# Optimization experiments

Hardware: AMD Instinct MI355X
Metric: run time of the kernel (lower is better)

The kernel has to match this reference:

```python
import jax, jax.numpy as jnp
import numpy as np

N_NODES = 50000
N_EDGES = 800000
N_GRAPHS = 128
HIDDEN = 64
HEADS = 2
OUT = 4
NEG_SLOPE = 0.2
ALPHA_FLAG = 0.05


def _gat_conv(x, src, dst, W, a_src, a_dst, b):
    # PyG GATConv, concat=False (mean over heads), self-loops already appended.
    N = x.shape[0]
    H, C = a_src.shape
    xh = (x @ W).reshape(N, H, C)                       # [N,H,C]
    s_src = (xh * a_src).sum(-1)                        # [N,H]
    s_dst = (xh * a_dst).sum(-1)                        # [N,H]
    e = s_src[src] + s_dst[dst]                         # [E,H]
    e = jnp.where(e > 0, e, NEG_SLOPE * e)              # LeakyReLU(0.2)
    emax = jax.ops.segment_max(e, dst, num_segments=N)  # per-dst softmax max
    emax = jnp.where(jnp.isfinite(emax), emax, 0.0)
    p = jnp.exp(e - emax[dst])
    denom = jax.ops.segment_sum(p, dst, num_segments=N)
    alpha = p / (denom[dst] + 1e-16)                    # [E,H]
    out = jax.ops.segment_sum(alpha[:, :, None] * xh[src], dst, num_segments=N)
    return out.mean(axis=1) + b                         # [N,HIDDEN]


def setup_inputs() -> dict:
    key = jax.random.key(0)
    ks = jax.random.split(key, 32)
    f = lambda k, shape, s=0.1: (jax.random.normal(k, shape) * s).astype(jnp.float32)
    inp = {}
    inp['x_all'] = jax.random.normal(ks[0], (N_NODES, 8), dtype=jnp.float32)
    inp['climber'] = jax.random.normal(ks[1], (N_GRAPHS, 4), dtype=jnp.float32)
    inp['edge_index'] = jax.random.randint(ks[2], (2, N_EDGES), 0, N_NODES)
    inp['batch'] = jnp.sort(jax.random.randint(ks[3], (N_NODES,), 0, N_GRAPHS))
    H = HIDDEN
    inp['W_in'] = f(ks[4], (6, H)); inp['b_in'] = jnp.zeros((H,), jnp.float32)
    inp['W_c'] = f(ks[5], (4, H)); inp['b_c'] = jnp.zeros((H,), jnp.float32)
    inp['W_f1'] = f(ks[6], (H, 2 * H)); inp['b_f1'] = jnp.zeros((2 * H,), jnp.float32)
    inp['W_f2'] = f(ks[7], (H, 2 * H)); inp['b_f2'] = jnp.zeros((2 * H,), jnp.float32)
    inp['W_g1'] = f(ks[8], (H, HEADS * H)); inp['a_src1'] = f(ks[9], (HEADS, H)); inp['a_dst1'] = f(ks[10], (HEADS, H)); inp['b_g1'] = jnp.zeros((H,), jnp.float32)
    inp['W_g2'] = f(ks[11], (H, HEADS * H)); inp['a_src2'] = f(ks[12], (HEADS, H)); inp['a_dst2'] = f(ks[13], (HEADS, H)); inp['b_g2'] = jnp.zeros((H,), jnp.float32)
    inp['W_cl1'] = f(ks[14], (H, H)); inp['b_cl1'] = jnp.zeros((H,), jnp.float32)
    inp['W_cl2'] = f(ks[15], (H, OUT)); inp['b_cl2'] = jnp.zeros((OUT,), jnp.float32)
    inp['W_fh1'] = f(ks[16], (2, 8), 0.001); inp['b_fh1'] = jnp.zeros((8,), jnp.float32)
    inp['W_fh2'] = f(ks[17], (8, OUT), 0.001); inp['b_fh2'] = jnp.zeros((OUT,), jnp.float32)
    return inp


def reference(x_all, climber, edge_index, batch, W_in, b_in, W_c, b_c,
              W_f1, b_f1, W_f2, b_f2,
              W_g1, a_src1, a_dst1, b_g1,
              W_g2, a_src2, a_dst2, b_g2,
              W_cl1, b_cl1, W_cl2, b_cl2,
              W_fh1, b_fh1, W_fh2, b_fh2):
    N = x_all.shape[0]
    flags = x_all[:, -2:]
    x = x_all[:, :-2]
    # climber embedding (eval mode -> dropout is identity)
    c = jax.nn.relu(climber @ W_c + b_c)                 # [G,H]
    x = x @ W_in + b_in                                  # [N,H]
    # FiLM 1
    gb = c @ W_f1 + b_f1
    gamma, beta = jnp.split(gb, 2, axis=-1)
    x = x * (1.0 + gamma[batch]) + beta[batch]
    # add self-loops (PyG GATConv default)
    loop = jnp.arange(N, dtype=edge_index.dtype)
    src = jnp.concatenate([edge_index[0], loop])
    dst = jnp.concatenate([edge_index[1], loop])
    x = jax.nn.relu(_gat_conv(x, src, dst, W_g1, a_src1, a_dst1, b_g1))
    # FiLM 2
    gb = c @ W_f2 + b_f2
    gamma, beta = jnp.split(gb, 2, axis=-1)
    x = x * (1.0 + gamma[batch]) + beta[batch]
    x = jax.nn.relu(_gat_conv(x, src, dst, W_g2, a_src2, a_dst2, b_g2))
    logits_main = jax.nn.relu(x @ W_cl1 + b_cl1) @ W_cl2 + b_cl2
    logits_flag = jax.nn.relu(flags @ W_fh1 + b_fh1) @ W_fh2 + b_fh2
    return logits_main + ALPHA_FLAG * logits_flag
```

## Files before the change

### kernel.cpp

```cpp
#include <hip/hip_runtime.h>
#include <hip/hip_fp16.h>

#define NEG_SLOPE 0.2f
#define ALPHA_FLAG 0.05f

typedef _Float16 h2t __attribute__((ext_vector_type(2)));
union h2u { unsigned u; h2t h; __half2 hh; float f; };
static __device__ __forceinline__ h2t u_as_h2(unsigned u) { h2u c; c.u = u; return c.h; }
static __device__ __forceinline__ float h2_as_f(__half2 h) { h2u c; c.hh = h; return c.f; }
static __device__ __forceinline__ h2t f_as_h2(float f) { h2u c; c.f = f; return c.h; }

static inline size_t align256(size_t x) { return (x + 255) & ~(size_t)255; }

__global__ void prep_kernel(const float* __restrict__ climber,
                            const float* __restrict__ W_c, const float* __restrict__ b_c,
                            const float* __restrict__ W_f1, const float* __restrict__ b_f1,
                            const float* __restrict__ W_f2, const float* __restrict__ b_f2,
                            float* __restrict__ gb1, float* __restrict__ gb2) {
    __shared__ float c_sh[64];
    int g = blockIdx.x, t = threadIdx.x;
    if (t < 64) {
        float acc = b_c[t];
#pragma unroll
        for (int k = 0; k < 4; ++k) acc = fmaf(climber[g * 4 + k], W_c[k * 64 + t], acc);
        c_sh[t] = fmaxf(acc, 0.f);
    }
    __syncthreads();
    float a1 = b_f1[t], a2 = b_f2[t];
#pragma unroll 8
    for (int h = 0; h < 64; ++h) {
        float cv = c_sh[h];
        a1 = fmaf(cv, W_f1[h * 128 + t], a1);
        a2 = fmaf(cv, W_f2[h * 128 + t], a2);
    }
    gb1[g * 128 + t] = a1;
    gb2[g * 128 + t] = a2;
}

__global__ void hist_kernel(const int* __restrict__ dst, int E, int* __restrict__ counts) {
    int i4 = (blockIdx.x * blockDim.x + threadIdx.x) * 4;
    if (i4 + 3 < E) {
        int4 d = *(const int4*)&dst[i4];
        atomicAdd(&counts[d.x], 1);
        atomicAdd(&counts[d.y], 1);
        atomicAdd(&counts[d.z], 1);
        atomicAdd(&counts[d.w], 1);
    } else {
        for (int u = 0; u < 4; ++u)
            if (i4 + u < E) atomicAdd(&counts[dst[i4 + u]], 1);
    }
}

#define SCAN_CHUNK 1024
__global__ void scan_partial_kernel(const int* __restrict__ counts, int* __restrict__ block_sums, int N) {
    __shared__ int sh[256];
    int b = blockIdx.x, t = threadIdx.x;
    int idx0 = b * SCAN_CHUNK + t * 4;
    int s = 0;
    if (idx0 + 3 < N) {
        int4 v = *(const int4*)&counts[idx0];
        s = v.x + v.y + v.z + v.w + 4;
    } else {
#pragma unroll
        for (int u = 0; u < 4; ++u) if (idx0 + u < N) s += counts[idx0 + u] + 1;
    }
    sh[t] = s;
    __syncthreads();
#pragma unroll
    for (int off = 128; off; off >>= 1) {
        if (t < off) sh[t] += sh[t + off];
        __syncthreads();
    }
    if (t == 0) block_sums[b] = sh[0];
}

__global__ void scan_final_kernel(const int* __restrict__ counts, const int* __restrict__ block_sums,
                                  int nb, int* __restrict__ row_ptr, int* __restrict__ fill, int N) {
    __shared__ int sh[256];
    __shared__ int base_sh;
    int b = blockIdx.x, t = threadIdx.x;
    if (t < 64) {
        int v = (t < nb && t < b) ? block_sums[t] : 0;
#pragma unroll
        for (int off = 32; off; off >>= 1) v += __shfl_xor(v, off);
        if (t == 0) base_sh = v;
    }
    int idx0 = b * SCAN_CHUNK + t * 4;
    int c[4];
    if (idx0 + 3 < N) {
        int4 v = *(const int4*)&counts[idx0];
        c[0] = v.x + 1; c[1] = v.y + 1; c[2] = v.z + 1; c[3] = v.w + 1;
    } else {
#pragma unroll
        for (int u = 0; u < 4; ++u) c[u] = (idx0 + u < N) ? counts[idx0 + u] + 1 : 0;
    }
    int s = c[0] + c[1] + c[2] + c[3];
    sh[t] = s;
    __syncthreads();
#pragma unroll
    for (int off = 1; off < 256; off <<= 1) {
        int add = (t >= off) ? sh[t - off] : 0;
        __syncthreads();
        sh[t] += add;
        __syncthreads();
    }
    int run = base_sh + sh[t] - s;
#pragma unroll
    for (int u = 0; u < 4; ++u) {
        if (idx0 + u < N) {
            row_ptr[idx0 + u] = run;
            fill[idx0 + u] = run;
            run += c[u];
            if (idx0 + u == N - 1) row_ptr[N] = run;
        }
    }
}

__global__ void scatter_kernel(const int* __restrict__ src, const int* __restrict__ dst,
                               int Eh, int N, int* __restrict__ fill, int* __restrict__ csr_src) {
    int t = blockIdx.x * blockDim.x + threadIdx.x;
    if (t < Eh) {
        int2 s2 = *(const int2*)&src[t * 2];
        int2 d2 = *(const int2*)&dst[t * 2];
        int p0 = atomicAdd(&fill[d2.x], 1); csr_src[p0] = s2.x;
        int p1 = atomicAdd(&fill[d2.y], 1); csr_src[p1] = s2.y;
    } else {
        int i = t - Eh;
        if (i < N) { int p = atomicAdd(&fill[i], 1); csr_src[p] = i; }
    }
}

#define XH_NB 32
__global__ __launch_bounds__(256, 4) void xh_kernel(
    const __half* __restrict__ xhalf, const float* __restrict__ W_g,
    const float* __restrict__ a_src, const float* __restrict__ a_dst,
    __half* __restrict__ xh, float* __restrict__ s_src, float* __restrict__ s_dst,
    int N, int in_mode,
    const float* __restrict__ x_all, const int* __restrict__ batch,
    const float* __restrict__ W_in, const float* __restrict__ b_in,
    const float* __restrict__ gb1) {
    __shared__ float x_sh[XH_NB * 64];
    __shared__ float win_sh[6 * 64 + 64];
    int t = threadIdx.x;
    int base = blockIdx.x * XH_NB;
    if (in_mode) {
        for (int i = t; i < 448; i += 256)
            win_sh[i] = (i < 384) ? W_in[i] : b_in[i - 384];
        __syncthreads();
        int nd = t >> 3;
        int jb = (t & 7) * 8;
        int n = base + nd;
        if (n < N) {
            float4 a = *(const float4*)&x_all[(size_t)n * 8];
            float2 b = *(const float2*)&x_all[(size_t)n * 8 + 4];
            float xa[6] = {a.x, a.y, a.z, a.w, b.x, b.y};
            int g = batch[n];
            const float* gbrow = &gb1[g * 128];
#pragma unroll
            for (int jj = 0; jj < 8; ++jj) {
                int j = jb + jj;
                float acc = win_sh[384 + j];
#pragma unroll
                for (int k = 0; k < 6; ++k) acc = fmaf(xa[k], win_sh[k * 64 + j], acc);
                x_sh[nd * 64 + j] = acc * (1.f + gbrow[j]) + gbrow[64 + j];
            }
        } else {
#pragma unroll
            for (int jj = 0; jj < 8; ++jj) x_sh[nd * 64 + jb + jj] = 0.f;
        }
    } else {
        int nvalid = N - base; if (nvalid > XH_NB) nvalid = XH_NB;
        int nhalves = nvalid * 64;
        int idx = t * 8;
        uint4 raw = make_uint4(0, 0, 0, 0);
        if (idx < nhalves) raw = *(const uint4*)&xhalf[(size_t)base * 64 + idx];
        float2 f0 = __half22float2(*(__half2*)&raw.x);
        float2 f1 = __half22float2(*(__half2*)&raw.y);
        float2 f2 = __half22float2(*(__half2*)&raw.z);
        float2 f3 = __half22float2(*(__half2*)&raw.w);
        x_sh[idx + 0] = f0.x; x_sh[idx + 1] = f0.y;
        x_sh[idx + 2] = f1.x; x_sh[idx + 3] = f1.y;
        x_sh[idx + 4] = f2.x; x_sh[idx + 5] = f2.y;
        x_sh[idx + 6] = f3.x; x_sh[idx + 7] = f3.y;
    }
    __syncthreads();
    int c = t & 63;
    int g = t >> 6;
    float acc0[8], acc1[8];
#pragma unroll
    for (int i = 0; i < 8; ++i) { acc0[i] = 0.f; acc1[i] = 0.f; }
    const float* W0 = W_g + c;
    const float* W1 = W_g + 64 + c;
#pragma unroll 2
    for (int k = 0; k < 64; k += 4) {
        float w0[4], w1[4];
#pragma unroll
        for (int u = 0; u < 4; ++u) { w0[u] = W0[(k + u) * 128]; w1[u] = W1[(k + u) * 128]; }
#pragma unroll
        for (int i = 0; i < 8; ++i) {
            float4 xv = *(const float4*)&x_sh[(g * 8 + i) * 64 + k];
            acc0[i] = fmaf(xv.x, w0[0], acc0[i]);
            acc0[i] = fmaf(xv.y, w0[1], acc0[i]);
            acc0[i] = fmaf(xv.z, w0[2], acc0[i]);
            acc0[i] = fmaf(xv.w, w0[3], acc0[i]);
            acc1[i] = fmaf(xv.x, w1[0], acc1[i]);
            acc1[i] = fmaf(xv.y, w1[1], acc1[i]);
            acc1[i] = fmaf(xv.z, w1[2], acc1[i]);
            acc1[i] = fmaf(xv.w, w1[3], acc1[i]);
        }
    }
    float as0 = a_src[c], ad0 = a_dst[c];
    float as1 = a_src[64 + c], ad1 = a_dst[64 + c];
#pragma unroll
    for (int i = 0; i < 8; ++i) {
        int n = base + g * 8 + i;
        float ps0 = acc0[i] * as0, pd0 = acc0[i] * ad0;
        float ps1 = acc1[i] * as1, pd1 = acc1[i] * ad1;
#pragma unroll
        for (int off = 32; off; off >>= 1) {
            ps0 += __shfl_xor(ps0, off); pd0 += __shfl_xor(pd0, off);
            ps1 += __shfl_xor(ps1, off); pd1 += __shfl_xor(pd1, off);
        }
        if (n < N) {
            if (c == 0) {
                s_src[n * 2 + 0] = ps0; s_src[n * 2 + 1] = ps1;
                s_dst[n * 2 + 0] = pd0; s_dst[n * 2 + 1] = pd1;
            }
            __half2 hv = __floats2half2_rn(acc0[i], acc1[i]);
            *(__half2*)&xh[(size_t)n * 128 + c * 2] = hv;
        }
    }
}

static __device__ __forceinline__ float dot2acc(unsigned xbits, h2t w, float acc) {
#if __has_builtin(__builtin_amdgcn_fdot2)
    return __builtin_amdgcn_fdot2(u_as_h2(xbits), w, acc, false);
#else
    h2u cx; cx.u = xbits;
    float2 xf = __half22float2(cx.hh);
    h2u cw; cw.h = w;
    float2 wf = __half22float2(cw.hh);
    return fmaf(xf.x, wf.x, fmaf(xf.y, wf.y, acc));
#endif
}

template <int MODE>
static __device__ __forceinline__ void agg_impl(
    const __half* __restrict__ xh, const float* __restrict__ s_src,
    const float* __restrict__ s_dst, const int* __restrict__ row_ptr,
    const int* __restrict__ csr_src, const float* __restrict__ b_g,
    const int* __restrict__ batch, const float* __restrict__ gb_film,
    __half* __restrict__ xout_h, int N,
    const float* __restrict__ x_all,
    const float* __restrict__ W_cl1, const float* __restrict__ b_cl1,
    const float* __restrict__ W_cl2, const float* __restrict__ b_cl2,
    const float* __restrict__ W_fh1, const float* __restrict__ b_fh1,
    const float* __restrict__ W_fh2, const float* __restrict__ b_fh2,
    float* __restrict__ out) {
    __shared__ float2 ps_sh[4][64];
    __shared__ float vh_sh[4][64];
    int lane = threadIdx.x & 63;
    int w = threadIdx.x >> 6;
    int n = (blockIdx.x * blockDim.x + threadIdx.x) >> 6;
    if (n >= N) return;
    int beg = row_ptr[n], end = row_ptr[n + 1];
    int deg = end - beg;
    float2 sd = *(const float2*)&s_dst[n * 2];
    const char* xhb = (const char*)xh;
    int sub = lane >> 4;
    unsigned q16 = (unsigned)(lane & 15) * 16u;
    float acc[4] = {0.f, 0.f, 0.f, 0.f};

    if (deg <= 64) {
        float p0 = 0.f, p1 = 0.f; unsigned sb = 0;
        if (lane < deg) {
            int s = csr_src[beg + lane];
            sb = (unsigned)s << 8;
            float2 ss = *(const float2*)&s_src[s * 2];
            float e0 = ss.x + sd.x, e1 = ss.y + sd.y;
            e0 = (e0 > 0.f) ? e0 : NEG_SLOPE * e0;
            e1 = (e1 > 0.f) ? e1 : NEG_SLOPE * e1;
            p0 = __expf(e0); p1 = __expf(e1);
        }
        float dp0 = p0, dp1 = p1;
#pragma unroll
        for (int off = 32; off; off >>= 1) {
            dp0 += __shfl_xor(dp0, off);
            dp1 += __shfl_xor(dp1, off);
        }
        float i0 = 0.5f / (dp0 + 1e-16f), i1 = 0.5f / (dp1 + 1e-16f);
        ps_sh[w][lane] = make_float2(h2_as_f(__floats2half2_rn(p0 * i0, p1 * i1)),
                                     __uint_as_float(sb));
        int mr = (deg + 3) & ~3;
        for (int j = 0; j < mr; j += 4) {
            float2 ps = ps_sh[w][j + sub];
            h2t wpk = f_as_h2(ps.x);
            unsigned voff = __float_as_uint(ps.y) + q16;
            uint4 hv = *(const uint4*)(xhb + voff);
            acc[0] = dot2acc(hv.x, wpk, acc[0]);
            acc[1] = dot2acc(hv.y, wpk, acc[1]);
            acc[2] = dot2acc(hv.z, wpk, acc[2]);
            acc[3] = dot2acc(hv.w, wpk, acc[3]);
        }
    } else {
        float dp0 = 0.f, dp1 = 0.f;
        for (int chunk = beg; chunk < end; chunk += 64) {
            int m = end - chunk; if (m > 64) m = 64;
            if (lane < m) {
                int s = csr_src[chunk + lane];
                float2 ss = *(const float2*)&s_src[s * 2];
                float e0 = ss.x + sd.x, e1 = ss.y + sd.y;
                e0 = (e0 > 0.f) ? e0 : NEG_SLOPE * e0;
                e1 = (e1 > 0.f) ? e1 : NEG_SLOPE * e1;
                dp0 += __expf(e0); dp1 += __expf(e1);
            }
        }
#pragma unroll
        for (int off = 32; off; off >>= 1) {
            dp0 += __shfl_xor(dp0, off);
            dp1 += __shfl_xor(dp1, off);
        }
        float i0 = 0.5f / (dp0 + 1e-16f), i1 = 0.5f / (dp1 + 1e-16f);
        for (int chunk = beg; chunk < end; chunk += 64) {
            int m = end - chunk; if (m > 64) m = 64;
            float p0 = 0.f, p1 = 0.f; unsigned sb = 0;
            if (lane < m) {
                int s = csr_src[chunk + lane];
                sb = (unsigned)s << 8;
                float2 ss = *(const float2*)&s_src[s * 2];
                float e0 = ss.x + sd.x, e1 = ss.y + sd.y;
                e0 = (e0 > 0.f) ? e0 : NEG_SLOPE * e0;
                e1 = (e1 > 0.f) ? e1 : NEG_SLOPE * e1;
                p0 = __expf(e0); p1 = __expf(e1);
            }
            ps_sh[w][lane] = make_float2(h2_as_f(__floats2half2_rn(p0 * i0, p1 * i1)),
                                         __uint_as_float(sb));
            int mr = (m + 3) & ~3;
            for (int j = 0; j < mr; j += 4) {
                float2 ps = ps_sh[w][j + sub];
                h2t wpk = f_as_h2(ps.x);
                unsigned voff = __float_as_uint(ps.y) + q16;
                uint4 hv = *(const uint4*)(xhb + voff);
                acc[0] = dot2acc(hv.x, wpk, acc[0]);
                acc[1] = dot2acc(hv.y, wpk, acc[1]);
                acc[2] = dot2acc(hv.z, wpk, acc[2]);
                acc[3] = dot2acc(hv.w, wpk, acc[3]);
            }
        }
    }
#pragma unroll
    for (int u = 0; u < 4; ++u) {
        acc[u] += __shfl_xor(acc[u], 16);
        acc[u] += __shfl_xor(acc[u], 32);
    }
    if (lane < 16) *(float4*)&vh_sh[w][lane * 4] = make_float4(acc[0], acc[1], acc[2], acc[3]);
    float v = vh_sh[w][lane] + b_g[lane];
    v = fmaxf(v, 0.f);
    if (MODE == 0) {
        int g = batch[n];
        v = v * (1.f + gb_film[g * 128 + lane]) + gb_film[g * 128 + 64 + lane];
        xout_h[(size_t)n * 64 + lane] = __float2half(v);
        return;
    }
    vh_sh[w][lane] = v;
    float h = b_cl1[lane];
#pragma unroll 4
    for (int k = 0; k < 64; k += 4) {
        float4 vq = *(const float4*)&vh_sh[w][k];
        h = fmaf(vq.x, W_cl1[(k + 0) * 64 + lane], h);
        h = fmaf(vq.y, W_cl1[(k + 1) * 64 + lane], h);
        h = fmaf(vq.z, W_cl1[(k + 2) * 64 + lane], h);
        h = fmaf(vq.w, W_cl1[(k + 3) * 64 + lane], h);
    }
    h = fmaxf(h, 0.f);
    float4 w2 = *(const float4*)&W_cl2[lane * 4];
    float o0 = h * w2.x, o1 = h * w2.y, o2 = h * w2.z, o3 = h * w2.w;
#pragma unroll
    for (int off = 32; off; off >>= 1) {
        o0 += __shfl_xor(o0, off); o1 += __shfl_xor(o1, off);
        o2 += __shfl_xor(o2, off); o3 += __shfl_xor(o3, off);
    }
    if (lane < 4) {
        float f0 = x_all[(size_t)n * 8 + 6], f1 = x_all[(size_t)n * 8 + 7];
        float lf = b_fh2[lane];
#pragma unroll
        for (int m = 0; m < 8; ++m) {
            float fm = fmaxf(fmaf(f0, W_fh1[m], fmaf(f1, W_fh1[8 + m], b_fh1[m])), 0.f);
            lf = fmaf(fm, W_fh2[m * 4 + lane], lf);
        }
        float om = (lane == 0) ? o0 : (lane == 1) ? o1 : (lane == 2) ? o2 : o3;
        out[(size_t)n * 4 + lane] = om + b_cl2[lane] + ALPHA_FLAG * lf;
    }
}

__global__ __launch_bounds__(256) void agg_film_kernel(
    const __half* xh, const float* s_src, const float* s_dst, const int* row_ptr,
    const int* csr_src, const float* b_g, const int* batch, const float* gb_film,
    __half* xout_h, int N) {
    agg_impl<0>(xh, s_src, s_dst, row_ptr, csr_src, b_g, batch, gb_film, xout_h, N,
                nullptr, nullptr, nullptr, nullptr, nullptr, nullptr, nullptr,
                nullptr, nullptr, nullptr);
}

__global__ __launch_bounds__(256) void agg_cls_kernel(
    const __half* xh, const float* s_src, const float* s_dst, const int* row_ptr,
    const int* csr_src, const float* b_g, int N, const float* x_all,
    const float* W_cl1, const float* b_cl1, const float* W_cl2, const float* b_cl2,
    const float* W_fh1, const float* b_fh1, const float* W_fh2, const float* b_fh2,
    float* out) {
    agg_impl<1>(xh, s_src, s_dst, row_ptr, csr_src, b_g, nullptr, nullptr, nullptr, N,
                x_all, W_cl1, b_cl1, W_cl2, b_cl2, W_fh1, b_fh1, W_fh2, b_fh2, out);
}

extern "C" void kernel_launch(void* const* d_in, const int* in_sizes, int n_in,
                              void* d_out, int out_size, void* d_ws, size_t ws_size,
                              hipStream_t stream) {
    const float* x_all   = (const float*)d_in[0];
    const float* climber = (const float*)d_in[1];
    const int*   eidx    = (const int*)d_in[2];
    const int*   batch   = (const int*)d_in[3];
    const float* W_in  = (const float*)d_in[4];
    const float* b_in  = (const float*)d_in[5];
    const float* W_c   = (const float*)d_in[6];
    const float* b_c   = (const float*)d_in[7];
    const float* W_f1  = (const float*)d_in[8];
    const float* b_f1  = (const float*)d_in[9];
    const float* W_f2  = (const float*)d_in[10];
    const float* b_f2  = (const float*)d_in[11];
    const float* W_g1  = (const float*)d_in[12];
    const float* a_s1  = (const float*)d_in[13];
    const float* a_d1  = (const float*)d_in[14];
    const float* b_g1  = (const float*)d_in[15];
    const float* W_g2  = (const float*)d_in[16];
    const float* a_s2  = (const float*)d_in[17];
    const float* a_d2  = (const float*)d_in[18];
    const float* b_g2  = (const float*)d_in[19];
    const float* W_cl1 = (const float*)d_in[20];
    const float* b_cl1 = (const float*)d_in[21];
    const float* W_cl2 = (const float*)d_in[22];
    const float* b_cl2 = (const float*)d_in[23];
    const float* W_fh1 = (const float*)d_in[24];
    const float* b_fh1 = (const float*)d_in[25];
    const float* W_fh2 = (const float*)d_in[26];
    const float* b_fh2 = (const float*)d_in[27];
    float* out = (float*)d_out;

    const int N = in_sizes[0] / 8;
    const int E = in_sizes[2] / 2;
    const int G = in_sizes[1] / 4;
    const int* src = eidx;
    const int* dst = eidx + E;
    const int NB_SCAN = (N + SCAN_CHUNK - 1) / SCAN_CHUNK;

    char* ws = (char*)d_ws;
    size_t off = 0;
    auto alloc = [&](size_t bytes) { char* p = ws + off; off += align256(bytes); return p; };
    float*  gb1     = (float*)alloc((size_t)G * 128 * 4);
    float*  gb2     = (float*)alloc((size_t)G * 128 * 4);
    __half* xbuf    = (__half*)alloc((size_t)N * 64 * 2);
    __half* xh      = (__half*)alloc((size_t)N * 128 * 2);
    float*  s_src   = (float*)alloc((size_t)N * 2 * 4);
    float*  s_dst   = (float*)alloc((size_t)N * 2 * 4);
    int*    counts  = (int*)alloc((size_t)N * 4);
    int*    fill    = (int*)alloc((size_t)N * 4);
    int*    row_ptr = (int*)alloc((size_t)(N + 1) * 4);
    int*    csr_src = (int*)alloc((size_t)(E + N) * 4);
    int*    bsums   = (int*)alloc((size_t)64 * 4);
    (void)ws_size;

    prep_kernel<<<G, 128, 0, stream>>>(climber, W_c, b_c, W_f1, b_f1, W_f2, b_f2, gb1, gb2);
    hipMemsetAsync(counts, 0, (size_t)N * 4, stream);
    hist_kernel<<<(E / 4 + 255) / 256, 256, 0, stream>>>(dst, E, counts);
    scan_partial_kernel<<<NB_SCAN, 256, 0, stream>>>(counts, bsums, N);
    scan_final_kernel<<<NB_SCAN, 256, 0, stream>>>(counts, bsums, NB_SCAN, row_ptr, fill, N);
    scatter_kernel<<<(E / 2 + N + 255) / 256, 256, 0, stream>>>(src, dst, E / 2, N, fill, csr_src);
    xh_kernel<<<(N + XH_NB - 1) / XH_NB, 256, 0, stream>>>(nullptr, W_g1, a_s1, a_d1, xh,
                                                           s_src, s_dst, N, 1,
                                                           x_all, batch, W_in, b_in, gb1);
    agg_film_kernel<<<(N * 64 + 255) / 256, 256, 0, stream>>>(xh, s_src, s_dst, row_ptr, csr_src,
                                                              b_g1, batch, gb2, xbuf, N);
    xh_kernel<<<(N + XH_NB - 1) / XH_NB, 256, 0, stream>>>(xbuf, W_g2, a_s2, a_d2, xh,
                                                           s_src, s_dst, N, 0,
                                                           nullptr, nullptr, nullptr, nullptr, nullptr);
    agg_cls_kernel<<<(N * 64 + 255) / 256, 256, 0, stream>>>(xh, s_src, s_dst, row_ptr, csr_src,
                                                             b_g2, N, x_all, W_cl1, b_cl1,
                                                             W_cl2, b_cl2, W_fh1, b_fh1,
                                                             W_fh2, b_fh2, out);
}
```

Baseline: 257.5 us.

## Fuse layer-1 aggregation with layer-2 linear projection and attention scores

Merges the first GAT aggregation plus FiLM with the second layer's x@W_g2 projection and s_src/s_dst score computation into one kernel, removing the intermediate half-precision x buffer round trip and one launch. Each block handles 4 nodes, and pairs of waves compute one head for two nodes, reading W_g2 straight from global memory. Separate xh/score buffers are used per layer to avoid read/write hazards. The fused projection has less weight reuse than the former 32-node tiled xh kernel and adds block-wide syncs, so the aggregation phase may lose some latency hiding.

```diff
diff --git a/kernel.cpp b/kernel.cpp
--- a/kernel.cpp
+++ b/kernel.cpp
@@ -131,11 +131,11 @@
 }
 
 #define XH_NB 32
-__global__ __launch_bounds__(256, 4) void xh_kernel(
-    const __half* __restrict__ xhalf, const float* __restrict__ W_g,
+__global__ __launch_bounds__(256, 4) void xh1_kernel(
+    const float* __restrict__ W_g,
     const float* __restrict__ a_src, const float* __restrict__ a_dst,
     __half* __restrict__ xh, float* __restrict__ s_src, float* __restrict__ s_dst,
-    int N, int in_mode,
+    int N,
     const float* __restrict__ x_all, const int* __restrict__ batch,
     const float* __restrict__ W_in, const float* __restrict__ b_in,
     const float* __restrict__ gb1) {
@@ -143,10 +143,10 @@
     __shared__ float win_sh[6 * 64 + 64];
     int t = threadIdx.x;
     int base = blockIdx.x * XH_NB;
-    if (in_mode) {
-        for (int i = t; i < 448; i += 256)
-            win_sh[i] = (i < 384) ? W_in[i] : b_in[i - 384];
-        __syncthreads();
+    for (int i = t; i < 448; i += 256)
+        win_sh[i] = (i < 384) ? W_in[i] : b_in[i - 384];
+    __syncthreads();
+    {
         int nd = t >> 3;
         int jb = (t & 7) * 8;
         int n = base + nd;
@@ -168,20 +168,6 @@
 #pragma unroll
             for (int jj = 0; jj < 8; ++jj) x_sh[nd * 64 + jb + jj] = 0.f;
         }
-    } else {
-        int nvalid = N - base; if (nvalid > XH_NB) nvalid = XH_NB;
-        int nhalves = nvalid * 64;
-        int idx = t * 8;
-        uint4 raw = make_uint4(0, 0, 0, 0);
-        if (idx < nhalves) raw = *(const uint4*)&xhalf[(size_t)base * 64 + idx];
-        float2 f0 = __half22float2(*(__half2*)&raw.x);
-        float2 f1 = __half22float2(*(__half2*)&raw.y);
-        float2 f2 = __half22float2(*(__half2*)&raw.z);
-        float2 f3 = __half22float2(*(__half2*)&raw.w);
-        x_sh[idx + 0] = f0.x; x_sh[idx + 1] = f0.y;
-        x_sh[idx + 2] = f1.x; x_sh[idx + 3] = f1.y;
-        x_sh[idx + 4] = f2.x; x_sh[idx + 5] = f2.y;
-        x_sh[idx + 6] = f3.x; x_sh[idx + 7] = f3.y;
     }
     __syncthreads();
     int c = t & 63;
@@ -244,28 +230,15 @@
 #endif
 }
 
-template <int MODE>
-static __device__ __forceinline__ void agg_impl(
+static __device__ __forceinline__ float agg_core(
     const __half* __restrict__ xh, const float* __restrict__ s_src,
     const float* __restrict__ s_dst, const int* __restrict__ row_ptr,
-    const int* __restrict__ csr_src, const float* __restrict__ b_g,
-    const int* __restrict__ batch, const float* __restrict__ gb_film,
-    __half* __restrict__ xout_h, int N,
-    const float* __restrict__ x_all,
-    const float* __restrict__ W_cl1, const float* __restrict__ b_cl1,
-    const float* __restrict__ W_cl2, const float* __restrict__ b_cl2,
-    const float* __restrict__ W_fh1, const float* __restrict__ b_fh1,
-    const float* __restrict__ W_fh2, const float* __restrict__ b_fh2,
-    float* __restrict__ out) {
-    __shared__ float2 ps_sh[4][64];
-    __shared__ float vh_sh[4][64];
-    int lane = threadIdx.x & 63;
-    int w = threadIdx.x >> 6;
-    int n = (blockIdx.x * blockDim.x + threadIdx.x) >> 6;
-    if (n >= N) return;
-    int beg = row_ptr[n], end = row_ptr[n + 1];
+    const int* __restrict__ csr_src, int n, int N, int lane, int w,
+    float2 (* __restrict__ ps_sh)[64], float (* __restrict__ vh_sh)[64]) {
+    int beg = 0, end = 0;
+    if (n < N) { beg = row_ptr[n]; end = row_ptr[n + 1]; }
     int deg = end - beg;
-    float2 sd = *(const float2*)&s_dst[n * 2];
+    float2 sd = (n < N) ? *(const float2*)&s_dst[n * 2] : make_float2(0.f, 0.f);
     const char* xhb = (const char*)xh;
     int sub = lane >> 4;
     unsigned q16 = (unsigned)(lane & 15) * 16u;
@@ -354,14 +327,93 @@
         acc[u] += __shfl_xor(acc[u], 32);
     }
     if (lane < 16) *(float4*)&vh_sh[w][lane * 4] = make_float4(acc[0], acc[1], acc[2], acc[3]);
-    float v = vh_sh[w][lane] + b_g[lane];
-    v = fmaxf(v, 0.f);
-    if (MODE == 0) {
+    return vh_sh[w][lane];
+}
+
+__global__ __launch_bounds__(256) void agg_film_xh_kernel(
+    const __half* __restrict__ xh1, const float* __restrict__ s_src1,
+    const float* __restrict__ s_dst1, const int* __restrict__ row_ptr,
+    const int* __restrict__ csr_src, const float* __restrict__ b_g1,
+    const int* __restrict__ batch, const float* __restrict__ gb2,
+    const float* __restrict__ W_g2, const float* __restrict__ a_src2,
+    const float* __restrict__ a_dst2,
+    __half* __restrict__ xh2, float* __restrict__ s_src2, float* __restrict__ s_dst2,
+    int N) {
+    __shared__ float2 ps_sh[4][64];
+    __shared__ float v_sh[4][64];
+    __shared__ __half xh_sh[4][128];
+    int t = threadIdx.x;
+    int lane = t & 63;
+    int w = t >> 6;
+    int node0 = blockIdx.x * 4;
+    int n = node0 + w;
+    float v = agg_core(xh1, s_src1, s_dst1, row_ptr, csr_src, n, N, lane, w, ps_sh, v_sh);
+    v = fmaxf(v + b_g1[lane], 0.f);
+    if (n < N) {
         int g = batch[n];
-        v = v * (1.f + gb_film[g * 128 + lane]) + gb_film[g * 128 + 64 + lane];
-        xout_h[(size_t)n * 64 + lane] = __float2half(v);
-        return;
-    }
+        v = v * (1.f + gb2[g * 128 + lane]) + gb2[g * 128 + 64 + lane];
+    }
+    v_sh[w][lane] = v;
+    __syncthreads();
+    int c = lane;
+    int h = w & 1;
+    int pr = w >> 1;
+    const float* Wc = W_g2 + h * 64 + c;
+    const float* vA = v_sh[2 * pr];
+    const float* vB = v_sh[2 * pr + 1];
+    float accA = 0.f, accB = 0.f;
+#pragma unroll 4
+    for (int k = 0; k < 64; k += 4) {
+        float w0 = Wc[(k + 0) * 128], w1 = Wc[(k + 1) * 128];
+        float w2 = Wc[(k + 2) * 128], w3 = Wc[(k + 3) * 128];
+        float4 a4 = *(const float4*)&vA[k];
+        float4 b4 = *(const float4*)&vB[k];
+        accA = fmaf(a4.x, w0, accA); accB = fmaf(b4.x, w0, accB);
+        accA = fmaf(a4.y, w1, accA); accB = fmaf(b4.y, w1, accB);
+        accA = fmaf(a4.z, w2, accA); accB = fmaf(b4.z, w2, accB);
+        accA = fmaf(a4.w, w3, accA); accB = fmaf(b4.w, w3, accB);
+    }
+    float as = a_src2[h * 64 + c], ad = a_dst2[h * 64 + c];
+    float psA = accA * as, pdA = accA * ad;
+    float psB = accB * as, pdB = accB * ad;
+#pragma unroll
+    for (int off = 32; off; off >>= 1) {
+        psA += __shfl_xor(psA, off); pdA += __shfl_xor(pdA, off);
+        psB += __shfl_xor(psB, off); pdB += __shfl_xor(pdB, off);
+    }
+    int nA = node0 + 2 * pr, nB = nA + 1;
+    if (lane == 0) {
+        if (nA < N) { s_src2[nA * 2 + h] = psA; s_dst2[nA * 2 + h] = pdA; }
+        if (nB < N) { s_src2[nB * 2 + h] = psB; s_dst2[nB * 2 + h] = pdB; }
+    }
+    xh_sh[2 * pr][c * 2 + h] = __float2half(accA);
+    xh_sh[2 * pr + 1][c * 2 + h] = __float2half(accB);
+    __syncthreads();
+    int nw = node0 + (t >> 6);
+    if (nw < N) {
+        unsigned val = ((const unsigned*)xh_sh)[t];
+        *(unsigned*)((char*)xh2 + (size_t)nw * 256 + (t & 63) * 4) = val;
+    }
+}
+
+__global__ __launch_bounds__(256) void agg_cls_kernel(
+    const __half* __restrict__ xh, const float* __restrict__ s_src,
+    const float* __restrict__ s_dst, const int* __restrict__ row_ptr,
+    const int* __restrict__ csr_src, const float* __restrict__ b_g, int N,
+    const float* __restrict__ x_all,
+    const float* __restrict__ W_cl1, const float* __restrict__ b_cl1,
+    const float* __restrict__ W_cl2, const float* __restrict__ b_cl2,
+    const float* __restrict__ W_fh1, const float* __restrict__ b_fh1,
+    const float* __restrict__ W_fh2, const float* __restrict__ b_fh2,
+    float* __restrict__ out) {
+    __shared__ float2 ps_sh[4][64];
+    __shared__ float vh_sh[4][64];
+    int lane = threadIdx.x & 63;
+    int w = threadIdx.x >> 6;
+    int n = (blockIdx.x * blockDim.x + threadIdx.x) >> 6;
+    if (n >= N) return;
+    float v = agg_core(xh, s_src, s_dst, row_ptr, csr_src, n, N, lane, w, ps_sh, vh_sh);
+    v = fmaxf(v + b_g[lane], 0.f);
     vh_sh[w][lane] = v;
     float h = b_cl1[lane];
 #pragma unroll 4
@@ -391,25 +443,6 @@
         float om = (lane == 0) ? o0 : (lane == 1) ? o1 : (lane == 2) ? o2 : o3;
         out[(size_t)n * 4 + lane] = om + b_cl2[lane] + ALPHA_FLAG * lf;
     }
-}
-
-__global__ __launch_bounds__(256) void agg_film_kernel(
-    const __half* xh, const float* s_src, const float* s_dst, const int* row_ptr,
-    const int* csr_src, const float* b_g, const int* batch, const float* gb_film,
-    __half* xout_h, int N) {
-    agg_impl<0>(xh, s_src, s_dst, row_ptr, csr_src, b_g, batch, gb_film, xout_h, N,
-                nullptr, nullptr, nullptr, nullptr, nullptr, nullptr, nullptr,
-                nullptr, nullptr, nullptr);
-}
-
-__global__ __launch_bounds__(256) void agg_cls_kernel(
-    const __half* xh, const float* s_src, const float* s_dst, const int* row_ptr,
-    const int* csr_src, const float* b_g, int N, const float* x_all,
-    const float* W_cl1, const float* b_cl1, const float* W_cl2, const float* b_cl2,
-    const float* W_fh1, const float* b_fh1, const float* W_fh2, const float* b_fh2,
-    float* out) {
-    agg_impl<1>(xh, s_src, s_dst, row_ptr, csr_src, b_g, nullptr, nullptr, nullptr, N,
-                x_all, W_cl1, b_cl1, W_cl2, b_cl2, W_fh1, b_fh1, W_fh2, b_fh2, out);
 }
 
 extern "C" void kernel_launch(void* const* d_in, const int* in_sizes, int n_in,
@@ -457,10 +490,12 @@
     auto alloc = [&](size_t bytes) { char* p = ws + off; off += align256(bytes); return p; };
     float*  gb1     = (float*)alloc((size_t)G * 128 * 4);
     float*  gb2     = (float*)alloc((size_t)G * 128 * 4);
-    __half* xbuf    = (__half*)alloc((size_t)N * 64 * 2);
-    __half* xh      = (__half*)alloc((size_t)N * 128 * 2);
-    float*  s_src   = (float*)alloc((size_t)N * 2 * 4);
-    float*  s_dst   = (float*)alloc((size_t)N * 2 * 4);
+    __half* xh1     = (__half*)alloc((size_t)N * 128 * 2);
+    __half* xh2     = (__half*)alloc((size_t)N * 128 * 2);
+    float*  s_src1  = (float*)alloc((size_t)N * 2 * 4);
+    float*  s_dst1  = (float*)alloc((size_t)N * 2 * 4);
+    float*  s_src2  = (float*)alloc((size_t)N * 2 * 4);
+    float*  s_dst2  = (float*)alloc((size_t)N * 2 * 4);
     int*    counts  = (int*)alloc((size_t)N * 4);
     int*    fill    = (int*)alloc((size_t)N * 4);
     int*    row_ptr = (int*)alloc((size_t)(N + 1) * 4);
@@ -474,15 +509,13 @@
     scan_partial_kernel<<<NB_SCAN, 256, 0, stream>>>(counts, bsums, N);
     scan_final_kernel<<<NB_SCAN, 256, 0, stream>>>(counts, bsums, NB_SCAN, row_ptr, fill, N);
     scatter_kernel<<<(E / 2 + N + 255) / 256, 256, 0, stream>>>(src, dst, E / 2, N, fill, csr_src);
-    xh_kernel<<<(N + XH_NB - 1) / XH_NB, 256, 0, stream>>>(nullptr, W_g1, a_s1, a_d1, xh,
-                                                           s_src, s_dst, N, 1,
-                                                           x_all, batch, W_in, b_in, gb1);
-    agg_film_kernel<<<(N * 64 + 255) / 256, 256, 0, stream>>>(xh, s_src, s_dst, row_ptr, csr_src,
-                                                              b_g1, batch, gb2, xbuf, N);
-    xh_kernel<<<(N + XH_NB - 1) / XH_NB, 256, 0, stream>>>(xbuf, W_g2, a_s2, a_d2, xh,
-                                                           s_src, s_dst, N, 0,
-                                                           nullptr, nullptr, nullptr, nullptr, nullptr);
-    agg_cls_kernel<<<(N * 64 + 255) / 256, 256, 0, stream>>>(xh, s_src, s_dst, row_ptr, csr_src,
+    xh1_kernel<<<(N + XH_NB - 1) / XH_NB, 256, 0, stream>>>(W_g1, a_s1, a_d1, xh1,
+                                                            s_src1, s_dst1, N,
+                                                            x_all, batch, W_in, b_in, gb1);
+    agg_film_xh_kernel<<<(N + 3) / 4, 256, 0, stream>>>(xh1, s_src1, s_dst1, row_ptr, csr_src,
+                                                        b_g1, batch, gb2, W_g2, a_s2, a_d2,
+                                                        xh2, s_src2, s_dst2, N);
+    agg_cls_kernel<<<(N * 64 + 255) / 256, 256, 0, stream>>>(xh2, s_src2, s_dst2, row_ptr, csr_src,
                                                              b_g2, N, x_all, W_cl1, b_cl1,
                                                              W_cl2, b_cl2, W_fh1, b_fh1,
                                                              W_fh2, b_fh2, out);
```

After: 262.9 us. 2.1% more time.

## Record edge ranks during histogram to drop scatter atomics and merge scan kernels

Applied to the files above, without the earlier changes.

The histogram pass now keeps the return value of each atomicAdd as a per-edge rank within its destination. The scatter pass then writes each edge to row_ptr[dst]+rank without a second round of atomics. The two-pass scan becomes a single kernel: each block recomputes its prefix by summing all earlier counts. This removes one launch and the contended scatter atomics, at the cost of an extra E-sized rank buffer and redundant prefix reads that grow with block index.

```diff
diff --git a/kernel.cpp b/kernel.cpp
--- a/kernel.cpp
+++ b/kernel.cpp
@@ -37,54 +37,41 @@
     gb2[g * 128 + t] = a2;
 }
 
-__global__ void hist_kernel(const int* __restrict__ dst, int E, int* __restrict__ counts) {
+__global__ void hist_kernel(const int* __restrict__ dst, int E,
+                            int* __restrict__ counts, int* __restrict__ ranks) {
     int i4 = (blockIdx.x * blockDim.x + threadIdx.x) * 4;
     if (i4 + 3 < E) {
         int4 d = *(const int4*)&dst[i4];
-        atomicAdd(&counts[d.x], 1);
-        atomicAdd(&counts[d.y], 1);
-        atomicAdd(&counts[d.z], 1);
-        atomicAdd(&counts[d.w], 1);
+        int4 r;
+        r.x = atomicAdd(&counts[d.x], 1);
+        r.y = atomicAdd(&counts[d.y], 1);
+        r.z = atomicAdd(&counts[d.z], 1);
+        r.w = atomicAdd(&counts[d.w], 1);
+        *(int4*)&ranks[i4] = r;
     } else {
         for (int u = 0; u < 4; ++u)
-            if (i4 + u < E) atomicAdd(&counts[dst[i4 + u]], 1);
+            if (i4 + u < E) ranks[i4 + u] = atomicAdd(&counts[dst[i4 + u]], 1);
     }
 }
 
 #define SCAN_CHUNK 1024
-__global__ void scan_partial_kernel(const int* __restrict__ counts, int* __restrict__ block_sums, int N) {
+__global__ void scan_kernel(const int* __restrict__ counts, int* __restrict__ row_ptr, int N) {
     __shared__ int sh[256];
     int b = blockIdx.x, t = threadIdx.x;
-    int idx0 = b * SCAN_CHUNK + t * 4;
-    int s = 0;
-    if (idx0 + 3 < N) {
-        int4 v = *(const int4*)&counts[idx0];
-        s = v.x + v.y + v.z + v.w + 4;
-    } else {
-#pragma unroll
-        for (int u = 0; u < 4; ++u) if (idx0 + u < N) s += counts[idx0 + u] + 1;
-    }
-    sh[t] = s;
+    int pre = 0;
+    for (int i0 = t * 4; i0 < b * SCAN_CHUNK; i0 += 1024) {
+        int4 v = *(const int4*)&counts[i0];
+        pre += v.x + v.y + v.z + v.w + 4;
+    }
+    sh[t] = pre;
     __syncthreads();
 #pragma unroll
     for (int off = 128; off; off >>= 1) {
         if (t < off) sh[t] += sh[t + off];
         __syncthreads();
     }
-    if (t == 0) block_sums[b] = sh[0];
-}
-
-__global__ void scan_final_kernel(const int* __restrict__ counts, const int* __restrict__ block_sums,
-                                  int nb, int* __restrict__ row_ptr, int* __restrict__ fill, int N) {
-    __shared__ int sh[256];
-    __shared__ int base_sh;
-    int b = blockIdx.x, t = threadIdx.x;
-    if (t < 64) {
-        int v = (t < nb && t < b) ? block_sums[t] : 0;
-#pragma unroll
-        for (int off = 32; off; off >>= 1) v += __shfl_xor(v, off);
-        if (t == 0) base_sh = v;
-    }
+    int base = sh[0];
+    __syncthreads();
     int idx0 = b * SCAN_CHUNK + t * 4;
     int c[4];
     if (idx0 + 3 < N) {
@@ -104,12 +91,11 @@
         sh[t] += add;
         __syncthreads();
     }
-    int run = base_sh + sh[t] - s;
+    int run = base + sh[t] - s;
 #pragma unroll
     for (int u = 0; u < 4; ++u) {
         if (idx0 + u < N) {
             row_ptr[idx0 + u] = run;
-            fill[idx0 + u] = run;
             run += c[u];
             if (idx0 + u == N - 1) row_ptr[N] = run;
         }
@@ -117,16 +103,19 @@
 }
 
 __global__ void scatter_kernel(const int* __restrict__ src, const int* __restrict__ dst,
-                               int Eh, int N, int* __restrict__ fill, int* __restrict__ csr_src) {
+                               const int* __restrict__ ranks, const int* __restrict__ counts,
+                               const int* __restrict__ row_ptr,
+                               int Eh, int N, int* __restrict__ csr_src) {
     int t = blockIdx.x * blockDim.x + threadIdx.x;
     if (t < Eh) {
         int2 s2 = *(const int2*)&src[t * 2];
         int2 d2 = *(const int2*)&dst[t * 2];
-        int p0 = atomicAdd(&fill[d2.x], 1); csr_src[p0] = s2.x;
-        int p1 = atomicAdd(&fill[d2.y], 1); csr_src[p1] = s2.y;
+        int2 r2 = *(const int2*)&ranks[t * 2];
+        csr_src[row_ptr[d2.x] + r2.x] = s2.x;
+        csr_src[row_ptr[d2.y] + r2.y] = s2.y;
     } else {
         int i = t - Eh;
-        if (i < N) { int p = atomicAdd(&fill[i], 1); csr_src[p] = i; }
+        if (i < N) csr_src[row_ptr[i] + counts[i]] = i;
     }
 }
 
@@ -462,18 +451,17 @@
     float*  s_src   = (float*)alloc((size_t)N * 2 * 4);
     float*  s_dst   = (float*)alloc((size_t)N * 2 * 4);
     int*    counts  = (int*)alloc((size_t)N * 4);
-    int*    fill    = (int*)alloc((size_t)N * 4);
+    int*    ranks   = (int*)alloc((size_t)E * 4);
     int*    row_ptr = (int*)alloc((size_t)(N + 1) * 4);
     int*    csr_src = (int*)alloc((size_t)(E + N) * 4);
-    int*    bsums   = (int*)alloc((size_t)64 * 4);
     (void)ws_size;
 
     prep_kernel<<<G, 128, 0, stream>>>(climber, W_c, b_c, W_f1, b_f1, W_f2, b_f2, gb1, gb2);
     hipMemsetAsync(counts, 0, (size_t)N * 4, stream);
-    hist_kernel<<<(E / 4 + 255) / 256, 256, 0, stream>>>(dst, E, counts);
-    scan_partial_kernel<<<NB_SCAN, 256, 0, stream>>>(counts, bsums, N);
-    scan_final_kernel<<<NB_SCAN, 256, 0, stream>>>(counts, bsums, NB_SCAN, row_ptr, fill, N);
-    scatter_kernel<<<(E / 2 + N + 255) / 256, 256, 0, stream>>>(src, dst, E / 2, N, fill, csr_src);
+    hist_kernel<<<(E / 4 + 255) / 256, 256, 0, stream>>>(dst, E, counts, ranks);
+    scan_kernel<<<NB_SCAN, 256, 0, stream>>>(counts, row_ptr, N);
+    scatter_kernel<<<(E / 2 + N + 255) / 256, 256, 0, stream>>>(src, dst, ranks, counts,
+                                                                row_ptr, E / 2, N, csr_src);
     xh_kernel<<<(N + XH_NB - 1) / XH_NB, 256, 0, stream>>>(nullptr, W_g1, a_s1, a_d1, xh,
                                                            s_src, s_dst, N, 1,
                                                            x_all, batch, W_in, b_in, gb1);
```

New measurement: 228.6 us. 11.2% less time.
